# Kernel tuning notes

Measured on AMD Instinct MI355X. Metric: run time of the kernel, lower is better.

## Reference

```python
import jax, jax.numpy as jnp
import numpy as np

B, S, D = 2, 2048, 2048
H, HKV = 32, 8
DH = D // H          # 64
G = H // HKV         # group size 4


def setup_inputs() -> dict:
    key = jax.random.key(0)
    ks = jax.random.split(key, 5)
    sc = lambda fan_in: 1.0 / np.sqrt(fan_in)
    return {
        "hidden_states": jax.random.normal(ks[0], (B, S, D), jnp.float32),
        "Wq": jax.random.normal(ks[1], (D, D), jnp.float32) * sc(D),
        "bq": jnp.zeros((D,), jnp.float32),
        "Wk": jax.random.normal(ks[2], (D, HKV * DH), jnp.float32) * sc(D),
        "bk": jnp.zeros((HKV * DH,), jnp.float32),
        "Wv": jax.random.normal(ks[3], (D, HKV * DH), jnp.float32) * sc(D),
        "bv": jnp.zeros((HKV * DH,), jnp.float32),
        "Wo": jax.random.normal(ks[4], (D, D), jnp.float32) * sc(D),
        "bo": jnp.zeros((D,), jnp.float32),
    }


def reference(hidden_states, Wq, bq, Wk, bk, Wv, bv, Wo, bo):
    x = hidden_states
    # projections
    q = x @ Wq + bq                     # [B,S,D]
    k = x @ Wk + bk                     # [B,S,HKV*DH]
    v = x @ Wv + bv
    # split heads; group queries so K/V broadcast instead of repeat_interleave
    # (same math: repeat_interleave expands kv head j to query heads j*G..j*G+G-1)
    q = q.reshape(B, S, HKV, G, DH).transpose(0, 2, 3, 1, 4)  # [B,HKV,G,S,DH]
    k = k.reshape(B, S, HKV, DH).transpose(0, 2, 1, 3)        # [B,HKV,S,DH]
    v = v.reshape(B, S, HKV, DH).transpose(0, 2, 1, 3)
    scale = 1.0 / jnp.sqrt(jnp.asarray(DH, q.dtype))
    scores = jnp.einsum('bhgqd,bhkd->bhgqk', q, k) * scale    # [B,HKV,G,S,S]
    attn = jax.nn.softmax(scores, axis=-1)
    ctx = jnp.einsum('bhgqk,bhkd->bhgqd', attn, v)            # [B,HKV,G,S,DH]
    # merge heads back to [B,S,D] (head order = kv_head*G + group idx)
    merged = ctx.transpose(0, 3, 1, 2, 4).reshape(B, S, D)
    out = merged @ Wo + bo
    return out
```

## Files before the change

kernel.cpp:

```cpp
#include <hip/hip_runtime.h>
#include <cstdint>

typedef __bf16 bf16;
typedef __attribute__((ext_vector_type(8))) __bf16 bf16x8;
typedef __attribute__((ext_vector_type(4))) __bf16 bf16x4;
typedef __attribute__((ext_vector_type(2))) __bf16 bf16x2;
typedef __attribute__((ext_vector_type(4))) float f32x4;
typedef __attribute__((ext_vector_type(16))) float f32x16;

#define B_   2
#define S_   2048
#define D_   2048
#define HKV_ 8
#define H_   32
#define DH_  64

__device__ __forceinline__ void async_cp16(const bf16* g, bf16* l) {
  __builtin_amdgcn_global_load_lds(
      (__attribute__((address_space(1))) void*)g,
      (__attribute__((address_space(3))) void*)l,
      16, 0, 0);
}

__device__ __forceinline__ float fexp2(float x) {
#if __has_builtin(__builtin_amdgcn_exp2f)
  return __builtin_amdgcn_exp2f(x);
#else
  return __expf(x * 0.69314718056f);
#endif
}

__global__ __launch_bounds__(256) void downcast_k(
    const float* __restrict__ in, bf16* __restrict__ out, int n8) {
  const int i = blockIdx.x * 256 + threadIdx.x;
  if (i < n8) {
    const float4* p = (const float4*)(in + (size_t)i * 8);
    const float4 lo = p[0];
    const float4 hi = p[1];
    bf16x8 v;
    v[0] = (bf16)lo.x; v[1] = (bf16)lo.y; v[2] = (bf16)lo.z; v[3] = (bf16)lo.w;
    v[4] = (bf16)hi.x; v[5] = (bf16)hi.y; v[6] = (bf16)hi.z; v[7] = (bf16)hi.w;
    *(bf16x8*)(out + (size_t)i * 8) = v;
  }
}

__global__ __launch_bounds__(256) void transpose_k(
    const float* __restrict__ in, bf16* __restrict__ out, int R, int C) {
  __shared__ bf16 tile[64][65];
  const int tx = threadIdx.x & 63;
  const int ty = threadIdx.x >> 6;
  const int r0 = blockIdx.x * 64;
  const int c0 = blockIdx.y * 64;
#pragma unroll
  for (int j = 0; j < 16; ++j) {
    int r = j * 4 + ty;
    tile[r][tx] = (bf16)in[(size_t)(r0 + r) * C + c0 + tx];
  }
  __syncthreads();
#pragma unroll
  for (int j = 0; j < 16; ++j) {
    int r = j * 4 + ty;
    out[(size_t)(c0 + r) * R + r0 + tx] = tile[tx][r];
  }
}

template <int OMODE>
__global__ __launch_bounds__(256) void gemm_bt(
    const bf16* __restrict__ A, const bf16* __restrict__ Bt,
    const float* __restrict__ b1, const float* __restrict__ b2,
    const float* __restrict__ b3,
    void* __restrict__ C0, void* __restrict__ C1, void* __restrict__ C2,
    int N, int K) {
  __shared__ bf16 a_tile[2][128 * 64];
  __shared__ bf16 b_tile[2][128 * 64];
  const int tid  = threadIdx.x;
  const int wave = tid >> 6;
  const int lane = tid & 63;
  const int quad = lane >> 4;
  const int l16  = lane & 15;

  const int nwg = gridDim.x * gridDim.y;
  const int id  = blockIdx.y * gridDim.x + blockIdx.x;
  const int per = nwg >> 3;
  const int sw  = (id & 7) * per + (id >> 3);
  const int m0  = (sw % gridDim.x) * 128;
  const int n0  = (sw / gridDim.x) * 128;

  f32x4 acc[4][4] = {};

  const int srow  = wave * 32 + (lane >> 3);
  const int skoff = (lane & 7) * 8;
  const bf16* Ag = A  + (size_t)(m0 + srow) * K + skoff;
  const bf16* Bg = Bt + (size_t)(n0 + srow) * K + skoff;
  bf16* al = &a_tile[0][srow * 64 + skoff];
  bf16* bl = &b_tile[0][srow * 64 + skoff];

  auto stage = [&](int buf, int kt) {
    const int bo = buf * 8192;
#pragma unroll
    for (int c = 0; c < 4; ++c)
      async_cp16(Ag + (size_t)(c * 8) * K + kt, al + bo + c * 512);
#pragma unroll
    for (int c = 0; c < 4; ++c)
      async_cp16(Bg + (size_t)(c * 8) * K + kt, bl + bo + c * 512);
  };

  stage(0, 0);
  __syncthreads();

  for (int kt = 0; kt < K; kt += 64) {
    const int cur = (kt >> 6) & 1;
    if (kt + 64 < K) stage(cur ^ 1, kt + 64);
    const bf16* at = &a_tile[cur][0];
    const bf16* bt = &b_tile[cur][0];
#pragma unroll
    for (int kk = 0; kk < 64; kk += 32) {
      bf16x8 af[4], bfr[4];
#pragma unroll
      for (int i = 0; i < 4; ++i) {
        af[i]  = *(const bf16x8*)&at[((wave >> 1) * 64 + i * 16 + l16) * 64 + kk + quad * 8];
        bfr[i] = *(const bf16x8*)&bt[((wave & 1) * 64 + i * 16 + l16) * 64 + kk + quad * 8];
      }
#pragma unroll
      for (int i = 0; i < 4; ++i)
#pragma unroll
        for (int j = 0; j < 4; ++j)
          acc[i][j] = __builtin_amdgcn_mfma_f32_16x16x32_bf16(af[i], bfr[j], acc[i][j], 0, 0, 0);
    }
    __syncthreads();
  }

  const int wm = (wave >> 1) * 64;
  const int wn = (wave & 1) * 64;
#pragma unroll
  for (int i = 0; i < 4; ++i) {
    const int row = m0 + wm + i * 16 + quad * 4;
#pragma unroll
    for (int j = 0; j < 4; ++j) {
      const int col = n0 + wn + j * 16 + l16;
      if constexpr (OMODE == 2) {
        const float bia = b1[col];
#pragma unroll
        for (int r = 0; r < 4; ++r)
          ((float*)C0)[(size_t)(row + r) * N + col] = acc[i][j][r] + bia;
      } else {
        if (col < 2048) {
          const float bia = b1[col];
#pragma unroll
          for (int r = 0; r < 4; ++r)
            ((bf16*)C0)[(size_t)(row + r) * 2048 + col] =
                (bf16)((acc[i][j][r] + bia) * 0.18033688f);
        } else if (col < 2560) {
          const int cc = col - 2048;
          const float bia = b2[cc];
#pragma unroll
          for (int r = 0; r < 4; ++r)
            ((bf16*)C1)[(size_t)(row + r) * 512 + cc] = (bf16)(acc[i][j][r] + bia);
        } else {
          const int cc = col - 2560;
          const float bia = b3[cc];
          const int hh = cc >> 6, dd = cc & 63;
#pragma unroll
          for (int r = 0; r < 4; ++r) {
            const int rr = row + r;
            const int bb = rr >> 11, ss = rr & 2047;
            ((bf16*)C2)[((((size_t)bb * HKV_ + hh) * DH_ + dd) << 11) + ss] =
                (bf16)(acc[i][j][r] + bia);
          }
        }
      }
    }
  }
}

__global__ __launch_bounds__(256, 2) void gqa_flash(
    const bf16* __restrict__ Qs,
    const bf16* __restrict__ Kb,
    const bf16* __restrict__ VT,
    bf16* __restrict__ ctx) {
  __shared__ bf16 k_tile[2][128 * 64];

  const int tid  = threadIdx.x;
  const int wave = tid >> 6;
  const int lane = tid & 63;
  const int l32  = lane & 31;
  const int hi   = lane >> 5;

  const int qt = blockIdx.x;
  const int hq = blockIdx.y;
  const int b  = blockIdx.z;
  const int h  = hq >> 2;

  const int r2 = (l32 & 7) ^ ((l32 >> 3) & 3);

  bf16x8 qf0[4], qf1[4];
  const int qrow0 = b * S_ + qt * 256 + wave * 64;
  {
    const bf16* qp = Qs + (size_t)(qrow0 + l32) * D_ + hq * DH_ + hi * 8;
#pragma unroll
    for (int ks = 0; ks < 4; ++ks) {
      qf0[ks] = *(const bf16x8*)(qp + ks * 16);
      qf1[ks] = *(const bf16x8*)(qp + (size_t)32 * D_ + ks * 16);
    }
  }

  f32x16 o0[2] = {}, o1[2] = {};
  float l_run0 = 0.f, l_run1 = 0.f;

  const int cg0 = (lane & 7) ^ ((lane >> 3) & 7);
  const bf16* Kg0 = Kb + (size_t)(b * S_ + wave * 32 + (lane >> 3)) * (HKV_ * DH_) + h * DH_;
  const int ldsl = wave * 2048 + lane * 8;

  const bf16* Vrow = VT + ((size_t)(b * HKV_ + h) * DH_ + l32) * S_ + hi * 8;

  auto stage = [&](int buf, int kt0) {
    bf16* kd = &k_tile[0][0] + buf * 8192 + ldsl;
#pragma unroll
    for (int c = 0; c < 4; ++c)
      async_cp16(Kg0 + (size_t)(kt0 + c * 8) * (HKV_ * DH_) + ((cg0 ^ c) << 3),
                 kd + c * 512);
  };

  stage(0, 0);
  __syncthreads();

  for (int kt = 0; kt < S_; kt += 128) {
    stage(((kt >> 7) + 1) & 1, (kt + 128) & (S_ - 1));
    const bf16* ktile = k_tile[(kt >> 7) & 1];

#pragma unroll
    for (int kb = 0; kb < 4; ++kb) {
      f32x16 st0 = {}, st1 = {};
      __builtin_amdgcn_s_setprio(1);
#pragma unroll
      for (int ks = 0; ks < 4; ++ks) {
        bf16x8 kf = *(const bf16x8*)&ktile[(kb * 32 + l32) * 64 +
                                           (((ks * 2 + hi) ^ r2) << 3)];
        st0 = __builtin_amdgcn_mfma_f32_32x32x16_bf16(kf, qf0[ks], st0, 0, 0, 0);
        st1 = __builtin_amdgcn_mfma_f32_32x32x16_bf16(kf, qf1[ks], st1, 0, 0, 0);
      }
      __builtin_amdgcn_s_setprio(0);

      const int koff = kt + kb * 32;
      bf16x8 av00 = *(const bf16x8*)(Vrow + koff);
      bf16x8 av01 = *(const bf16x8*)(Vrow + (size_t)32 * S_ + koff);
      bf16x8 av10 = *(const bf16x8*)(Vrow + koff + 16);
      bf16x8 av11 = *(const bf16x8*)(Vrow + (size_t)32 * S_ + koff + 16);

#pragma unroll
      for (int kqlo = 0; kqlo < 2; ++kqlo) {
        int wa[4], wb[4];
        float sm0 = 0.f, sm1 = 0.f;
#pragma unroll
        for (int e2 = 0; e2 < 4; ++e2) {
          const int e = 4 * kqlo + e2;
          const float a0 = fexp2(st0[2 * e]);
          const float a1 = fexp2(st0[2 * e + 1]);
          sm0 += a0 + a1;
          bf16x2 t0; t0[0] = (bf16)a0; t0[1] = (bf16)a1;
          wa[e2] = __builtin_bit_cast(int, t0);
          const float c0 = fexp2(st1[2 * e]);
          const float c1 = fexp2(st1[2 * e + 1]);
          sm1 += c0 + c1;
          bf16x2 t1; t1[0] = (bf16)c0; t1[1] = (bf16)c1;
          wb[e2] = __builtin_bit_cast(int, t1);
        }
        l_run0 += sm0;
        l_run1 += sm1;

        auto ra0 = __builtin_amdgcn_permlane32_swap(wa[0], wa[2], false, false);
        auto ra1 = __builtin_amdgcn_permlane32_swap(wa[1], wa[3], false, false);
        auto rb0 = __builtin_amdgcn_permlane32_swap(wb[0], wb[2], false, false);
        auto rb1 = __builtin_amdgcn_permlane32_swap(wb[1], wb[3], false, false);
        union { int wi[4]; bf16x8 v; } pb0, pb1;
        pb0.wi[0] = ra0[0]; pb0.wi[1] = ra1[0]; pb0.wi[2] = ra0[1]; pb0.wi[3] = ra1[1];
        pb1.wi[0] = rb0[0]; pb1.wi[1] = rb1[0]; pb1.wi[2] = rb0[1]; pb1.wi[3] = rb1[1];

        const bf16x8 av0 = (kqlo == 0) ? av00 : av10;
        const bf16x8 av1 = (kqlo == 0) ? av01 : av11;
        __builtin_amdgcn_s_setprio(1);
        o0[0] = __builtin_amdgcn_mfma_f32_32x32x16_bf16(av0, pb0.v, o0[0], 0, 0, 0);
        o1[0] = __builtin_amdgcn_mfma_f32_32x32x16_bf16(av0, pb1.v, o1[0], 0, 0, 0);
        o0[1] = __builtin_amdgcn_mfma_f32_32x32x16_bf16(av1, pb0.v, o0[1], 0, 0, 0);
        o1[1] = __builtin_amdgcn_mfma_f32_32x32x16_bf16(av1, pb1.v, o1[1], 0, 0, 0);
        __builtin_amdgcn_s_setprio(0);
      }
    }
    __syncthreads();
  }

  l_run0 += __shfl_xor(l_run0, 32);
  l_run1 += __shfl_xor(l_run1, 32);
  const float inv0 = 1.f / l_run0;
  const float inv1 = 1.f / l_run1;

  const size_t qrowA = (size_t)(qrow0 + l32);
  const size_t qrowB = qrowA + 32;
#pragma unroll
  for (int jm = 0; jm < 2; ++jm)
#pragma unroll
    for (int c = 0; c < 4; ++c) {
      bf16x4 ov;
#pragma unroll
      for (int j = 0; j < 4; ++j) ov[j] = (bf16)(o0[jm][4 * c + j] * inv0);
      const int dh0 = jm * 32 + c * 8 + hi * 4;
      *(bf16x4*)&ctx[qrowA * D_ + hq * DH_ + dh0] = ov;
#pragma unroll
      for (int j = 0; j < 4; ++j) ov[j] = (bf16)(o1[jm][4 * c + j] * inv1);
      *(bf16x4*)&ctx[qrowB * D_ + hq * DH_ + dh0] = ov;
    }
}

extern "C" void kernel_launch(void* const* d_in, const int* in_sizes, int n_in,
                              void* d_out, int out_size, void* d_ws, size_t ws_size,
                              hipStream_t stream) {
  const float* x  = (const float*)d_in[0];
  const float* Wq = (const float*)d_in[1];
  const float* bq = (const float*)d_in[2];
  const float* Wk = (const float*)d_in[3];
  const float* bk = (const float*)d_in[4];
  const float* Wv = (const float*)d_in[5];
  const float* bv = (const float*)d_in[6];
  const float* Wo = (const float*)d_in[7];
  const float* bo = (const float*)d_in[8];
  float* out = (float*)d_out;

  char* ws = (char*)d_ws;
  bf16* WT  = (bf16*)(ws);
  bf16* ctx = (bf16*)(ws);
  bf16* WoT = (bf16*)(ws + 16777216);
  bf16* Qs  = (bf16*)(ws + 25165824);
  bf16* Kb  = (bf16*)(ws + 41943040);
  bf16* VT  = (bf16*)(ws + 46137344);
  bf16* xb  = (bf16*)d_out;

  dim3 blk(256);
  downcast_k<<<dim3(4096), blk, 0, stream>>>(x, xb, (B_ * S_ * D_) / 8);
  transpose_k<<<dim3(32, 32), blk, 0, stream>>>(Wq, WT, 2048, 2048);
  transpose_k<<<dim3(32, 8),  blk, 0, stream>>>(Wk, WT + (size_t)2048 * 2048, 2048, 512);
  transpose_k<<<dim3(32, 8),  blk, 0, stream>>>(Wv, WT + (size_t)2560 * 2048, 2048, 512);
  transpose_k<<<dim3(32, 32), blk, 0, stream>>>(Wo, WoT, 2048, 2048);

  gemm_bt<3><<<dim3(32, 24), blk, 0, stream>>>(
      xb, WT, bq, bk, bv, Qs, Kb, VT, 3072, 2048);

  gqa_flash<<<dim3(8, 32, 2), blk, 0, stream>>>(Qs, Kb, VT, ctx);

  gemm_bt<2><<<dim3(32, 16), blk, 0, stream>>>(
      ctx, WoT, bo, nullptr, nullptr, out, nullptr, nullptr, 2048, 2048);
}
```

Measured before the change: 379.9 us.

## Software-pipeline QK^T and softmax/PV across key blocks; drop GEMM tile swizzle

The attention inner loop now computes QK^T scores for the next 32-key block while the softmax and PV MFMAs of the previous block run, using double-buffered score registers. This lets MFMA work overlap with the exp/convert/permute VALU work. Separately, the GEMM kernel drops its XCD-aware block-index swizzle and maps blocks directly to tiles, which may change L2 locality across chiplets. The extra live score registers raise VGPR pressure and could reduce occupancy.

```diff
diff --git a/kernel.cpp b/kernel.cpp
--- a/kernel.cpp
+++ b/kernel.cpp
@@ -78,13 +78,8 @@
   const int lane = tid & 63;
   const int quad = lane >> 4;
   const int l16  = lane & 15;
-
-  const int nwg = gridDim.x * gridDim.y;
-  const int id  = blockIdx.y * gridDim.x + blockIdx.x;
-  const int per = nwg >> 3;
-  const int sw  = (id & 7) * per + (id >> 3);
-  const int m0  = (sw % gridDim.x) * 128;
-  const int n0  = (sw / gridDim.x) * 128;
+  const int m0   = blockIdx.x * 128;
+  const int n0   = blockIdx.y * 128;
 
   f32x4 acc[4][4] = {};
 
@@ -221,6 +216,66 @@
                  kd + c * 512);
   };
 
+  auto qk_step = [&](const bf16* ktile, int kb, f32x16& s0, f32x16& s1) {
+    f32x16 a = {}, c = {};
+    __builtin_amdgcn_s_setprio(1);
+#pragma unroll
+    for (int ks = 0; ks < 4; ++ks) {
+      bf16x8 kf = *(const bf16x8*)&ktile[(kb * 32 + l32) * 64 +
+                                         (((ks * 2 + hi) ^ r2) << 3)];
+      a = __builtin_amdgcn_mfma_f32_32x32x16_bf16(kf, qf0[ks], a, 0, 0, 0);
+      c = __builtin_amdgcn_mfma_f32_32x32x16_bf16(kf, qf1[ks], c, 0, 0, 0);
+    }
+    __builtin_amdgcn_s_setprio(0);
+    s0 = a; s1 = c;
+  };
+
+  auto sm_pv = [&](int koff, const f32x16& st0, const f32x16& st1) {
+    bf16x8 av00 = *(const bf16x8*)(Vrow + koff);
+    bf16x8 av01 = *(const bf16x8*)(Vrow + (size_t)32 * S_ + koff);
+    bf16x8 av10 = *(const bf16x8*)(Vrow + koff + 16);
+    bf16x8 av11 = *(const bf16x8*)(Vrow + (size_t)32 * S_ + koff + 16);
+
+#pragma unroll
+    for (int kqlo = 0; kqlo < 2; ++kqlo) {
+      int wa[4], wb[4];
+      float sm0 = 0.f, sm1 = 0.f;
+#pragma unroll
+      for (int e2 = 0; e2 < 4; ++e2) {
+        const int e = 4 * kqlo + e2;
+        const float a0 = fexp2(st0[2 * e]);
+        const float a1 = fexp2(st0[2 * e + 1]);
+        sm0 += a0 + a1;
+        bf16x2 t0; t0[0] = (bf16)a0; t0[1] = (bf16)a1;
+        wa[e2] = __builtin_bit_cast(int, t0);
+        const float c0 = fexp2(st1[2 * e]);
+        const float c1 = fexp2(st1[2 * e + 1]);
+        sm1 += c0 + c1;
+        bf16x2 t1; t1[0] = (bf16)c0; t1[1] = (bf16)c1;
+        wb[e2] = __builtin_bit_cast(int, t1);
+      }
+      l_run0 += sm0;
+      l_run1 += sm1;
+
+      auto ra0 = __builtin_amdgcn_permlane32_swap(wa[0], wa[2], false, false);
+      auto ra1 = __builtin_amdgcn_permlane32_swap(wa[1], wa[3], false, false);
+      auto rb0 = __builtin_amdgcn_permlane32_swap(wb[0], wb[2], false, false);
+      auto rb1 = __builtin_amdgcn_permlane32_swap(wb[1], wb[3], false, false);
+      union { int wi[4]; bf16x8 v; } pb0, pb1;
+      pb0.wi[0] = ra0[0]; pb0.wi[1] = ra1[0]; pb0.wi[2] = ra0[1]; pb0.wi[3] = ra1[1];
+      pb1.wi[0] = rb0[0]; pb1.wi[1] = rb1[0]; pb1.wi[2] = rb0[1]; pb1.wi[3] = rb1[1];
+
+      const bf16x8 av0 = (kqlo == 0) ? av00 : av10;
+      const bf16x8 av1 = (kqlo == 0) ? av01 : av11;
+      __builtin_amdgcn_s_setprio(1);
+      o0[0] = __builtin_amdgcn_mfma_f32_32x32x16_bf16(av0, pb0.v, o0[0], 0, 0, 0);
+      o1[0] = __builtin_amdgcn_mfma_f32_32x32x16_bf16(av0, pb1.v, o1[0], 0, 0, 0);
+      o0[1] = __builtin_amdgcn_mfma_f32_32x32x16_bf16(av1, pb0.v, o0[1], 0, 0, 0);
+      o1[1] = __builtin_amdgcn_mfma_f32_32x32x16_bf16(av1, pb1.v, o1[1], 0, 0, 0);
+      __builtin_amdgcn_s_setprio(0);
+    }
+  };
+
   stage(0, 0);
   __syncthreads();
 
@@ -228,64 +283,16 @@
     stage(((kt >> 7) + 1) & 1, (kt + 128) & (S_ - 1));
     const bf16* ktile = k_tile[(kt >> 7) & 1];
 
-#pragma unroll
-    for (int kb = 0; kb < 4; ++kb) {
-      f32x16 st0 = {}, st1 = {};
-      __builtin_amdgcn_s_setprio(1);
-#pragma unroll
-      for (int ks = 0; ks < 4; ++ks) {
-        bf16x8 kf = *(const bf16x8*)&ktile[(kb * 32 + l32) * 64 +
-                                           (((ks * 2 + hi) ^ r2) << 3)];
-        st0 = __builtin_amdgcn_mfma_f32_32x32x16_bf16(kf, qf0[ks], st0, 0, 0, 0);
-        st1 = __builtin_amdgcn_mfma_f32_32x32x16_bf16(kf, qf1[ks], st1, 0, 0, 0);
-      }
-      __builtin_amdgcn_s_setprio(0);
-
-      const int koff = kt + kb * 32;
-      bf16x8 av00 = *(const bf16x8*)(Vrow + koff);
-      bf16x8 av01 = *(const bf16x8*)(Vrow + (size_t)32 * S_ + koff);
-      bf16x8 av10 = *(const bf16x8*)(Vrow + koff + 16);
-      bf16x8 av11 = *(const bf16x8*)(Vrow + (size_t)32 * S_ + koff + 16);
-
-#pragma unroll
-      for (int kqlo = 0; kqlo < 2; ++kqlo) {
-        int wa[4], wb[4];
-        float sm0 = 0.f, sm1 = 0.f;
-#pragma unroll
-        for (int e2 = 0; e2 < 4; ++e2) {
-          const int e = 4 * kqlo + e2;
-          const float a0 = fexp2(st0[2 * e]);
-          const float a1 = fexp2(st0[2 * e + 1]);
-          sm0 += a0 + a1;
-          bf16x2 t0; t0[0] = (bf16)a0; t0[1] = (bf16)a1;
-          wa[e2] = __builtin_bit_cast(int, t0);
-          const float c0 = fexp2(st1[2 * e]);
-          const float c1 = fexp2(st1[2 * e + 1]);
-          sm1 += c0 + c1;
-          bf16x2 t1; t1[0] = (bf16)c0; t1[1] = (bf16)c1;
-          wb[e2] = __builtin_bit_cast(int, t1);
-        }
-        l_run0 += sm0;
-        l_run1 += sm1;
-
-        auto ra0 = __builtin_amdgcn_permlane32_swap(wa[0], wa[2], false, false);
-        auto ra1 = __builtin_amdgcn_permlane32_swap(wa[1], wa[3], false, false);
-        auto rb0 = __builtin_amdgcn_permlane32_swap(wb[0], wb[2], false, false);
-        auto rb1 = __builtin_amdgcn_permlane32_swap(wb[1], wb[3], false, false);
-        union { int wi[4]; bf16x8 v; } pb0, pb1;
-        pb0.wi[0] = ra0[0]; pb0.wi[1] = ra1[0]; pb0.wi[2] = ra0[1]; pb0.wi[3] = ra1[1];
-        pb1.wi[0] = rb0[0]; pb1.wi[1] = rb1[0]; pb1.wi[2] = rb0[1]; pb1.wi[3] = rb1[1];
-
-        const bf16x8 av0 = (kqlo == 0) ? av00 : av10;
-        const bf16x8 av1 = (kqlo == 0) ? av01 : av11;
-        __builtin_amdgcn_s_setprio(1);
-        o0[0] = __builtin_amdgcn_mfma_f32_32x32x16_bf16(av0, pb0.v, o0[0], 0, 0, 0);
-        o1[0] = __builtin_amdgcn_mfma_f32_32x32x16_bf16(av0, pb1.v, o1[0], 0, 0, 0);
-        o0[1] = __builtin_amdgcn_mfma_f32_32x32x16_bf16(av1, pb0.v, o0[1], 0, 0, 0);
-        o1[1] = __builtin_amdgcn_mfma_f32_32x32x16_bf16(av1, pb1.v, o1[1], 0, 0, 0);
-        __builtin_amdgcn_s_setprio(0);
-      }
-    }
+    f32x16 sA0, sA1, sB0, sB1;
+    qk_step(ktile, 0, sA0, sA1);
+    qk_step(ktile, 1, sB0, sB1);
+    sm_pv(kt +  0, sA0, sA1);
+    qk_step(ktile, 2, sA0, sA1);
+    sm_pv(kt + 32, sB0, sB1);
+    qk_step(ktile, 3, sB0, sB1);
+    sm_pv(kt + 64, sA0, sA1);
+    sm_pv(kt + 96, sB0, sB1);
+
     __syncthreads();
   }
 
```

Result: no change. 373.4 us (-1.7%).
